# Kernel optimization log

Measured on AMD Instinct MI355X. Metric: run time of the kernel, lower is better.

## Reference

```python
import jax, jax.numpy as jnp
import numpy as np

LN_EPS = 1e-5


def setup_inputs() -> dict:
    key = jax.random.key(0)
    ks = jax.random.split(key, 8)
    dim = 256
    b, n3 = 8, 6144  # seq dim holds 3 concatenated token streams of n=2048 each
    s = 0.02
    return {
        "x": jax.random.normal(ks[0], (b, n3, dim), jnp.float32),
        "ln_g": jnp.ones((dim,), jnp.float32),
        "ln_b": jnp.zeros((dim,), jnp.float32),
        "Wq": jax.random.normal(ks[1], (dim, dim), jnp.float32) * s,
        "bq": jax.random.normal(ks[2], (dim,), jnp.float32) * s,
        "Wk": jax.random.normal(ks[3], (dim, dim), jnp.float32) * s,
        "bk": jax.random.normal(ks[4], (dim,), jnp.float32) * s,
        "Wv": jax.random.normal(ks[5], (dim, dim), jnp.float32) * s,
        "bv": jax.random.normal(ks[6], (dim,), jnp.float32) * s,
        "Wo": jax.random.normal(ks[7], (dim, dim), jnp.float32) * s,
        "bo": jnp.zeros((dim,), jnp.float32),
        "heads": 8,
    }


def reference(x, ln_g, ln_b, Wq, bq, Wk, bk, Wv, bv, Wo, bo, heads):
    dim = x.shape[-1]
    scale = dim ** (-0.5)  # NOTE: full dim, as in the original module
    d = dim // heads

    def cross_attn(xcat):
        # LayerNorm over last dim (applied to concatenated [2b, n, dim])
        mu = jnp.mean(xcat, axis=-1, keepdims=True)
        var = jnp.mean(jnp.square(xcat - mu), axis=-1, keepdims=True)
        xn = (xcat - mu) * jax.lax.rsqrt(var + LN_EPS) * ln_g + ln_b
        x1, x2 = jnp.split(xn, 2, axis=0)  # queries from stream 1, kv from stream 2
        q = x1 @ Wq.T + bq
        k = x2 @ Wk.T + bk
        v = x2 @ Wv.T + bv
        b_, n_ = q.shape[0], q.shape[1]
        q = q.reshape(b_, n_, heads, d).transpose(0, 2, 1, 3)  # b h n d
        k = k.reshape(b_, n_, heads, d).transpose(0, 2, 1, 3)
        v = v.reshape(b_, n_, heads, d).transpose(0, 2, 1, 3)
        dots = jnp.einsum('bhid,bhjd->bhij', q, k) * scale
        attn = jax.nn.softmax(dots, axis=-1)
        out = jnp.einsum('bhij,bhjd->bhid', attn, v)
        out = out.transpose(0, 2, 1, 3).reshape(b_, n_, dim)
        return out @ Wo.T + bo  # dropout is identity in eval

    x_origin, x_emap, x_lbp = jnp.split(x, 3, axis=1)
    out_oe = cross_attn(jnp.concatenate((x_origin, x_emap), axis=0))
    out_ol = cross_attn(jnp.concatenate((x_origin, x_lbp), axis=0))
    return out_oe + out_ol
```

## Files before the change

### kernel.cpp

```cpp
#include <hip/hip_runtime.h>
#include <hip/hip_bf16.h>
#include <math.h>

#define LN_EPS 1e-5f
#define QSCALE 0.09016844005556021f

typedef __attribute__((ext_vector_type(8))) short short8;
typedef __attribute__((ext_vector_type(4))) short short4v;
typedef __attribute__((ext_vector_type(4))) float f32x4;

__device__ inline ushort f2bf(float f) {
  __hip_bfloat16 h = __float2bfloat16(f);
  return *reinterpret_cast<ushort*>(&h);
}

__device__ inline uint pk2bf(float a, float b) {
  uint ua = __float_as_uint(a) + 0x8000u;
  uint ub = __float_as_uint(b) + 0x8000u;
  return __builtin_amdgcn_perm(ub, ua, 0x07060302u);
}


__global__ __launch_bounds__(256) void ln_wcast_kernel(
    const float* __restrict__ x, const float* __restrict__ lng,
    const float* __restrict__ lnb,
    const float* __restrict__ Wq, const float* __restrict__ Wk,
    const float* __restrict__ Wv, const float* __restrict__ Wo,
    ushort* __restrict__ xn, ushort* __restrict__ wbf) {
  if (blockIdx.x < 256) {
    int t = blockIdx.x * 256 + threadIdx.x;
    int e0 = t * 4;
    int m = e0 >> 16, off = e0 & 65535;
    const float* src = (m == 0) ? Wq : (m == 1) ? Wk : (m == 2) ? Wv : Wo;
    float4 v = *(const float4*)(src + off);
    ushort4 o;
    o.x = f2bf(v.x); o.y = f2bf(v.y); o.z = f2bf(v.z); o.w = f2bf(v.w);
    *(ushort4*)(wbf + m * 65536 + off) = o;
    return;
  }
  int w = threadIdx.x >> 6;
  int lane = threadIdx.x & 63;
  size_t token = (size_t)(blockIdx.x - 256) * 4 + w;
  float4 v = *(const float4*)(x + token * 256 + lane * 4);
  float s  = v.x + v.y + v.z + v.w;
  float s2 = v.x * v.x + v.y * v.y + v.z * v.z + v.w * v.w;
#pragma unroll
  for (int off = 32; off >= 1; off >>= 1) {
    s  += __shfl_xor(s, off, 64);
    s2 += __shfl_xor(s2, off, 64);
  }
  float mu  = s * (1.0f / 256.0f);
  float var = s2 * (1.0f / 256.0f) - mu * mu;
  float rs  = rsqrtf(var + LN_EPS);
  float4 g = *(const float4*)(lng + lane * 4);
  float4 bb = *(const float4*)(lnb + lane * 4);
  ushort4 o;
  o.x = f2bf((v.x - mu) * rs * g.x + bb.x);
  o.y = f2bf((v.y - mu) * rs * g.y + bb.y);
  o.z = f2bf((v.z - mu) * rs * g.z + bb.z);
  o.w = f2bf((v.w - mu) * rs * g.w + bb.w);
  *(ushort4*)(xn + token * 256 + lane * 4) = o;
}

__global__ __launch_bounds__(256) void proj_kernel(
    const ushort* __restrict__ xn,
    const ushort* __restrict__ wq, const ushort* __restrict__ wk,
    const ushort* __restrict__ wv,
    const float* __restrict__ bq, const float* __restrict__ bk,
    const float* __restrict__ bv,
    ushort* __restrict__ qb, ushort* __restrict__ keb, ushort* __restrict__ vTe,
    ushort* __restrict__ klb, ushort* __restrict__ vTl) {
  int z = blockIdx.z;
  int tid = threadIdx.x;
  int w = tid >> 6, lane = tid & 63;
  int n = lane & 15, quad = lane >> 4;
  int cbase = blockIdx.y * 128 + w * 32;
  int b = (blockIdx.x * 128) >> 11;
  int r0 = (blockIdx.x * 128) & 2047;

  if (z == 0) {
    const ushort* xbase = xn + ((size_t)b * 6144 + r0) * 256;
    short8 wf[2][8];
#pragma unroll
    for (int ct = 0; ct < 2; ++ct)
#pragma unroll
      for (int kc = 0; kc < 8; ++kc)
        wf[ct][kc] = *(const short8*)(wq + (size_t)(cbase + ct * 16 + n) * 256 + kc * 32 + quad * 8);
    float4 bt[2];
    bt[0] = *(const float4*)(bq + cbase + quad * 4);
    bt[1] = *(const float4*)(bq + cbase + 16 + quad * 4);

    short8 xfA[8], xfB[8];
#pragma unroll
    for (int kc = 0; kc < 8; ++kc)
      xfA[kc] = *(const short8*)(xbase + (size_t)n * 256 + kc * 32 + quad * 8);

#pragma unroll
    for (int tt = 0; tt < 8; ++tt) {
      const short8* cur = (tt & 1) ? xfB : xfA;
      short8* nxt = (tt & 1) ? xfA : xfB;
      if (tt < 7) {
#pragma unroll
        for (int kc = 0; kc < 8; ++kc)
          nxt[kc] = *(const short8*)(xbase + (size_t)((tt + 1) * 16 + n) * 256 + kc * 32 + quad * 8);
      }
      f32x4 acc[2] = {{0.f, 0.f, 0.f, 0.f}, {0.f, 0.f, 0.f, 0.f}};
#pragma unroll
      for (int ct = 0; ct < 2; ++ct)
#pragma unroll
        for (int kc = 0; kc < 8; ++kc)
          acc[ct] = __builtin_amdgcn_mfma_f32_16x16x32_bf16(wf[ct][kc], cur[kc], acc[ct], 0, 0, 0);
      int n2 = r0 + tt * 16 + n;
#pragma unroll
      for (int ct = 0; ct < 2; ++ct) {
        int c = cbase + ct * 16 + quad * 4;
        int h = c >> 5, d = c & 31;
        float* bp = (float*)&bt[ct];
        ushort4 st;
        st.x = f2bf((acc[ct][0] + bp[0]) * QSCALE);
        st.y = f2bf((acc[ct][1] + bp[1]) * QSCALE);
        st.z = f2bf((acc[ct][2] + bp[2]) * QSCALE);
        st.w = f2bf((acc[ct][3] + bp[3]) * QSCALE);
        *(ushort4*)(qb + (((size_t)(b * 8 + h) * 2048) + n2) * 32 + d) = st;
      }
    }
  } else {
    int s = z;
    ushort* kout = (z == 1) ? keb : klb;
    ushort* vout = (z == 1) ? vTe : vTl;
    const ushort* xbase = xn + ((size_t)b * 6144 + s * 2048 + r0) * 256;
    short8 wfk[2][8], wfv[2][8];
#pragma unroll
    for (int ct = 0; ct < 2; ++ct)
#pragma unroll
      for (int kc = 0; kc < 8; ++kc) {
        wfk[ct][kc] = *(const short8*)(wk + (size_t)(cbase + ct * 16 + n) * 256 + kc * 32 + quad * 8);
        wfv[ct][kc] = *(const short8*)(wv + (size_t)(cbase + ct * 16 + n) * 256 + kc * 32 + quad * 8);
      }
    float4 btk[2];
    btk[0] = *(const float4*)(bk + cbase + quad * 4);
    btk[1] = *(const float4*)(bk + cbase + 16 + quad * 4);
    float bsv[2] = {bv[cbase + n], bv[cbase + 16 + n]};

    short8 xfA[8], xfB[8];
#pragma unroll
    for (int kc = 0; kc < 8; ++kc)
      xfA[kc] = *(const short8*)(xbase + (size_t)n * 256 + kc * 32 + quad * 8);

#pragma unroll
    for (int tt = 0; tt < 8; ++tt) {
      const short8* cur = (tt & 1) ? xfB : xfA;
      short8* nxt = (tt & 1) ? xfA : xfB;
      if (tt < 7) {
#pragma unroll
        for (int kc = 0; kc < 8; ++kc)
          nxt[kc] = *(const short8*)(xbase + (size_t)((tt + 1) * 16 + n) * 256 + kc * 32 + quad * 8);
      }
      f32x4 ack[2] = {{0.f, 0.f, 0.f, 0.f}, {0.f, 0.f, 0.f, 0.f}};
      f32x4 acv[2] = {{0.f, 0.f, 0.f, 0.f}, {0.f, 0.f, 0.f, 0.f}};
#pragma unroll
      for (int ct = 0; ct < 2; ++ct)
#pragma unroll
        for (int kc = 0; kc < 8; ++kc) {
          ack[ct] = __builtin_amdgcn_mfma_f32_16x16x32_bf16(wfk[ct][kc], cur[kc], ack[ct], 0, 0, 0);
          acv[ct] = __builtin_amdgcn_mfma_f32_16x16x32_bf16(cur[kc], wfv[ct][kc], acv[ct], 0, 0, 0);
        }
      int n2 = r0 + tt * 16 + n;
#pragma unroll
      for (int ct = 0; ct < 2; ++ct) {
        int c = cbase + ct * 16 + quad * 4;
        int h = c >> 5, d = c & 31;
        float* bp = (float*)&btk[ct];
        ushort4 st;
        st.x = f2bf(ack[ct][0] + bp[0]);
        st.y = f2bf(ack[ct][1] + bp[1]);
        st.z = f2bf(ack[ct][2] + bp[2]);
        st.w = f2bf(ack[ct][3] + bp[3]);
        *(ushort4*)(kout + (((size_t)(b * 8 + h) * 2048) + n2) * 32 + d) = st;
      }
      int tq = r0 + tt * 16 + quad * 4;
      int tile = tq >> 6, within = tq & 63;
#pragma unroll
      for (int ct = 0; ct < 2; ++ct) {
        int c = cbase + ct * 16 + n;
        int h = c >> 5, d = c & 31;
        ushort4 st;
        st.x = f2bf(acv[ct][0] + bsv[ct]);
        st.y = f2bf(acv[ct][1] + bsv[ct]);
        st.z = f2bf(acv[ct][2] + bsv[ct]);
        st.w = f2bf(acv[ct][3] + bsv[ct]);
        *(ushort4*)(vout + (size_t)(b * 8 + h) * 65536 + tile * 2048 + d * 64 + within) = st;
      }
    }
  }
}

__global__ __launch_bounds__(256) void attn_kernel(
    const ushort* __restrict__ q,
    const ushort* __restrict__ ke, const ushort* __restrict__ vTe,
    const ushort* __restrict__ kl, const ushort* __restrict__ vTl,
    ushort* __restrict__ osum) {
  __shared__ __align__(16) short Vt[4][32 * 72];

  int tid = threadIdx.x;
  int w = tid >> 6, lane = tid & 63;
  int n = lane & 15, quad = lane >> 4;
  short* VtW = &Vt[w][0];

  union { uint2 u; short4v s; } one_u;
  one_u.u.x = 0x3F803F80u; one_u.u.y = 0x3F803F80u;
  const short4v vone = one_u.s;

  int L = blockIdx.y * 8 + blockIdx.x;
  int xcd = L & 7, idx = L >> 3;
  int bh = (idx & 7) * 8 + xcd;
  int q0 = (idx >> 3) * 256;
  int qbase = q0 + w * 64;

  short8 qfrag[4];
#pragma unroll
  for (int gq = 0; gq < 4; ++gq)
    qfrag[gq] = *(const short8*)(q + ((size_t)bh * 2048 + qbase + gq * 16 + n) * 32 + quad * 8);

  f32x4 out_acc[4][2];
#pragma unroll
  for (int gq = 0; gq < 4; ++gq)
#pragma unroll
    for (int dh = 0; dh < 2; ++dh) out_acc[gq][dh] = (f32x4){0.f, 0.f, 0.f, 0.f};

  int vrow = lane >> 3, vcol = (lane & 7) * 8;

  for (int s = 0; s < 2; ++s) {
    const ushort* K  = (s == 0 ? ke : kl) + (size_t)bh * 2048 * 32;
    const ushort* VT = (s == 0 ? vTe : vTl) + (size_t)bh * 32 * 2048;
    f32x4 lacc[4];
    f32x4 oacc[4][2];
#pragma unroll
    for (int gq = 0; gq < 4; ++gq) {
      lacc[gq] = (f32x4){0.f, 0.f, 0.f, 0.f};
#pragma unroll
      for (int dh = 0; dh < 2; ++dh) oacc[gq][dh] = (f32x4){0.f, 0.f, 0.f, 0.f};
    }

    short8 kfc[4], vrc[4], kfn[4], vrn[4];
#pragma unroll
    for (int t4 = 0; t4 < 4; ++t4)
      kfc[t4] = *(const short8*)(K + (size_t)(t4 * 16 + n) * 32 + quad * 8);
#pragma unroll
    for (int it = 0; it < 4; ++it)
      vrc[it] = *(const short8*)(VT + it * 512 + vrow * 64 + vcol);

    for (int jt = 0; jt < 32; ++jt) {
      if (jt < 31) {
        size_t tb = (size_t)(jt + 1) * 2048;
#pragma unroll
        for (int t4 = 0; t4 < 4; ++t4)
          kfn[t4] = *(const short8*)(K + tb + (size_t)(t4 * 16 + n) * 32 + quad * 8);
#pragma unroll
        for (int it = 0; it < 4; ++it)
          vrn[it] = *(const short8*)(VT + tb + it * 512 + vrow * 64 + vcol);
      }
#pragma unroll
      for (int it = 0; it < 4; ++it)
        *(short8*)&VtW[(it * 8 + vrow) * 72 + vcol] = vrc[it];
      short4v vbf[2][4];
#pragma unroll
      for (int dh = 0; dh < 2; ++dh)
#pragma unroll
        for (int t4 = 0; t4 < 4; ++t4)
          vbf[dh][t4] = *(const short4v*)&VtW[(dh * 16 + n) * 72 + t4 * 16 + quad * 4];

#pragma unroll
      for (int gq = 0; gq < 4; ++gq) {
        f32x4 sacc[4];
#pragma unroll
        for (int t4 = 0; t4 < 4; ++t4) {
          f32x4 z = {0.f, 0.f, 0.f, 0.f};
          sacc[t4] = __builtin_amdgcn_mfma_f32_16x16x32_bf16(kfc[t4], qfrag[gq], z, 0, 0, 0);
        }
        short4v pf[4];
#pragma unroll
        for (int t4 = 0; t4 < 4; ++t4) {
          float p0 = __builtin_amdgcn_exp2f(sacc[t4][0]);
          float p1 = __builtin_amdgcn_exp2f(sacc[t4][1]);
          float p2 = __builtin_amdgcn_exp2f(sacc[t4][2]);
          float p3 = __builtin_amdgcn_exp2f(sacc[t4][3]);
          union { uint2 u; short4v s4; } cv;
          cv.u.x = pk2bf(p0, p1);
          cv.u.y = pk2bf(p2, p3);
          pf[t4] = cv.s4;
        }
#pragma unroll
        for (int t4 = 0; t4 < 4; ++t4) {
          oacc[gq][0] = __builtin_amdgcn_mfma_f32_16x16x16bf16_1k(
              pf[t4], vbf[0][t4], oacc[gq][0], 0, 0, 0);
          oacc[gq][1] = __builtin_amdgcn_mfma_f32_16x16x16bf16_1k(
              pf[t4], vbf[1][t4], oacc[gq][1], 0, 0, 0);
          lacc[gq] = __builtin_amdgcn_mfma_f32_16x16x16bf16_1k(
              pf[t4], vone, lacc[gq], 0, 0, 0);
        }
      }
#pragma unroll
      for (int t4 = 0; t4 < 4; ++t4) { kfc[t4] = kfn[t4]; }
#pragma unroll
      for (int it = 0; it < 4; ++it) { vrc[it] = vrn[it]; }
    }
#pragma unroll
    for (int gq = 0; gq < 4; ++gq) {
      f32x4 inv;
#pragma unroll
      for (int r = 0; r < 4; ++r) inv[r] = __builtin_amdgcn_rcpf(lacc[gq][r]);
#pragma unroll
      for (int dh = 0; dh < 2; ++dh)
        out_acc[gq][dh] += oacc[gq][dh] * inv;
    }
  }

  int b = bh >> 3, h = bh & 7;
#pragma unroll
  for (int gq = 0; gq < 4; ++gq)
#pragma unroll
    for (int dh = 0; dh < 2; ++dh) {
      f32x4 v = out_acc[gq][dh];
#pragma unroll
      for (int r = 0; r < 4; ++r) {
        size_t row = (size_t)b * 2048 + qbase + gq * 16 + quad * 4 + r;
        osum[row * 256 + h * 32 + dh * 16 + n] = f2bf(v[r]);
      }
    }
}

__global__ __launch_bounds__(256) void outproj_kernel(
    const ushort* __restrict__ osum, const ushort* __restrict__ wo,
    const float* __restrict__ bo, float* __restrict__ out) {
  int tid = threadIdx.x;
  int w = tid >> 6, lane = tid & 63;
  int n = lane & 15, quad = lane >> 4;
  int cbase = blockIdx.y * 128 + w * 32;

  short8 wfrag[2][8];
#pragma unroll
  for (int ct = 0; ct < 2; ++ct)
#pragma unroll
    for (int kc = 0; kc < 8; ++kc)
      wfrag[ct][kc] = *(const short8*)(wo + (size_t)(cbase + ct * 16 + n) * 256 + kc * 32 + quad * 8);
  float4 bt[2];
  bt[0] = *(const float4*)(bo + cbase + quad * 4);
  bt[1] = *(const float4*)(bo + cbase + 16 + quad * 4);

  const ushort* abase = osum + (size_t)(blockIdx.x * 128) * 256;
  short8 xfA[8], xfB[8];
#pragma unroll
  for (int kc = 0; kc < 8; ++kc)
    xfA[kc] = *(const short8*)(abase + (size_t)n * 256 + kc * 32 + quad * 8);

#pragma unroll
  for (int tt = 0; tt < 8; ++tt) {
    const short8* cur = (tt & 1) ? xfB : xfA;
    short8* nxt = (tt & 1) ? xfA : xfB;
    if (tt < 7) {
#pragma unroll
      for (int kc = 0; kc < 8; ++kc)
        nxt[kc] = *(const short8*)(abase + (size_t)((tt + 1) * 16 + n) * 256 + kc * 32 + quad * 8);
    }
    int tok = blockIdx.x * 128 + tt * 16 + n;
    f32x4 acc[2] = {{0.f, 0.f, 0.f, 0.f}, {0.f, 0.f, 0.f, 0.f}};
#pragma unroll
    for (int ct = 0; ct < 2; ++ct)
#pragma unroll
      for (int kc = 0; kc < 8; ++kc)
        acc[ct] = __builtin_amdgcn_mfma_f32_16x16x32_bf16(wfrag[ct][kc], cur[kc], acc[ct], 0, 0, 0);
#pragma unroll
    for (int ct = 0; ct < 2; ++ct) {
      int c = cbase + ct * 16 + quad * 4;
      float* bp = (float*)&bt[ct];
      float4 st;
      st.x = acc[ct][0] + 2.0f * bp[0];
      st.y = acc[ct][1] + 2.0f * bp[1];
      st.z = acc[ct][2] + 2.0f * bp[2];
      st.w = acc[ct][3] + 2.0f * bp[3];
      *(float4*)(out + (size_t)tok * 256 + c) = st;
    }
  }
}

extern "C" void kernel_launch(void* const* d_in, const int* in_sizes, int n_in,
                              void* d_out, int out_size, void* d_ws, size_t ws_size,
                              hipStream_t stream) {
  const float* x   = (const float*)d_in[0];
  const float* lng = (const float*)d_in[1];
  const float* lnb = (const float*)d_in[2];
  const float* Wq  = (const float*)d_in[3];
  const float* bq  = (const float*)d_in[4];
  const float* Wk  = (const float*)d_in[5];
  const float* bk  = (const float*)d_in[6];
  const float* Wv  = (const float*)d_in[7];
  const float* bv  = (const float*)d_in[8];
  const float* Wo  = (const float*)d_in[9];
  const float* bo  = (const float*)d_in[10];
  float* out = (float*)d_out;

  ushort* ws = (ushort*)d_ws;
  const size_t XN  = (size_t)49152 * 256;
  const size_t QKV = (size_t)64 * 2048 * 32;
  ushort* xn   = ws;
  ushort* wbf  = xn + XN;
  ushort* qb   = wbf + 4 * 65536;
  ushort* keb  = qb  + QKV;
  ushort* vTe  = keb + QKV;
  ushort* klb  = vTe + QKV;
  ushort* vTl  = klb + QKV;
  ushort* osum = vTl + QKV;

  hipLaunchKernelGGL(ln_wcast_kernel, dim3(12544), dim3(256), 0, stream,
                     x, lng, lnb, Wq, Wk, Wv, Wo, xn, wbf);
  hipLaunchKernelGGL(proj_kernel, dim3(128, 2, 3), dim3(256), 0, stream,
                     xn, wbf, wbf + 65536, wbf + 131072, bq, bk, bv,
                     qb, keb, vTe, klb, vTl);
  hipLaunchKernelGGL(attn_kernel, dim3(8, 64), dim3(256), 0, stream,
                     qb, keb, vTe, klb, vTl, osum);
  hipLaunchKernelGGL(outproj_kernel, dim3(128, 2), dim3(256), 0, stream,
                     osum, wbf + 196608, bo, out);
}
```

Measured before the change: 286.4 us.

## Store V pre-swizzled into MFMA fragment order and halve per-block query tile

After: 290.8 us. Within noise of the previous version (+1.5%).

```diff
diff --git a/kernel.cpp b/kernel.cpp
--- a/kernel.cpp
+++ b/kernel.cpp
@@ -179,33 +179,34 @@
         *(ushort4*)(kout + (((size_t)(b * 8 + h) * 2048) + n2) * 32 + d) = st;
       }
       int tq = r0 + tt * 16 + quad * 4;
-      int tile = tq >> 6, within = tq & 63;
+      int tile = tq >> 6;
+      int t4 = (tq >> 4) & 3;
+      int qp = (tq >> 2) & 3;
 #pragma unroll
       for (int ct = 0; ct < 2; ++ct) {
         int c = cbase + ct * 16 + n;
         int h = c >> 5, d = c & 31;
+        int dh = d >> 4, np = d & 15;
         ushort4 st;
         st.x = f2bf(acv[ct][0] + bsv[ct]);
         st.y = f2bf(acv[ct][1] + bsv[ct]);
         st.z = f2bf(acv[ct][2] + bsv[ct]);
         st.w = f2bf(acv[ct][3] + bsv[ct]);
-        *(ushort4*)(vout + (size_t)(b * 8 + h) * 65536 + tile * 2048 + d * 64 + within) = st;
+        *(ushort4*)(vout + (size_t)(b * 8 + h) * 65536
+                    + (size_t)((((tile * 2 + dh) * 4 + t4) * 64 + qp * 16 + np) * 4)) = st;
       }
     }
   }
 }
 
-__global__ __launch_bounds__(256) void attn_kernel(
+__global__ __launch_bounds__(256, 3) void attn_kernel(
     const ushort* __restrict__ q,
     const ushort* __restrict__ ke, const ushort* __restrict__ vTe,
     const ushort* __restrict__ kl, const ushort* __restrict__ vTl,
     ushort* __restrict__ osum) {
-  __shared__ __align__(16) short Vt[4][32 * 72];
-
   int tid = threadIdx.x;
   int w = tid >> 6, lane = tid & 63;
   int n = lane & 15, quad = lane >> 4;
-  short* VtW = &Vt[w][0];
 
   union { uint2 u; short4v s; } one_u;
   one_u.u.x = 0x3F803F80u; one_u.u.y = 0x3F803F80u;
@@ -214,41 +215,42 @@
   int L = blockIdx.y * 8 + blockIdx.x;
   int xcd = L & 7, idx = L >> 3;
   int bh = (idx & 7) * 8 + xcd;
-  int q0 = (idx >> 3) * 256;
-  int qbase = q0 + w * 64;
-
-  short8 qfrag[4];
-#pragma unroll
-  for (int gq = 0; gq < 4; ++gq)
+  int q0 = (idx >> 3) * 128;
+  int qbase = q0 + w * 32;
+
+  short8 qfrag[2];
+#pragma unroll
+  for (int gq = 0; gq < 2; ++gq)
     qfrag[gq] = *(const short8*)(q + ((size_t)bh * 2048 + qbase + gq * 16 + n) * 32 + quad * 8);
 
-  f32x4 out_acc[4][2];
-#pragma unroll
-  for (int gq = 0; gq < 4; ++gq)
-#pragma unroll
-    for (int dh = 0; dh < 2; ++dh) out_acc[gq][dh] = (f32x4){0.f, 0.f, 0.f, 0.f};
-
-  int vrow = lane >> 3, vcol = (lane & 7) * 8;
+  f32x4 outv[2][2];
+#pragma unroll
+  for (int gq = 0; gq < 2; ++gq)
+#pragma unroll
+    for (int dh = 0; dh < 2; ++dh) outv[gq][dh] = (f32x4){0.f, 0.f, 0.f, 0.f};
 
   for (int s = 0; s < 2; ++s) {
     const ushort* K  = (s == 0 ? ke : kl) + (size_t)bh * 2048 * 32;
-    const ushort* VT = (s == 0 ? vTe : vTl) + (size_t)bh * 32 * 2048;
-    f32x4 lacc[4];
-    f32x4 oacc[4][2];
-#pragma unroll
-    for (int gq = 0; gq < 4; ++gq) {
+    const ushort* VT = (s == 0 ? vTe : vTl) + (size_t)bh * 65536;
+    f32x4 lacc[2];
+    f32x4 oacc[2][2];
+#pragma unroll
+    for (int gq = 0; gq < 2; ++gq) {
       lacc[gq] = (f32x4){0.f, 0.f, 0.f, 0.f};
 #pragma unroll
       for (int dh = 0; dh < 2; ++dh) oacc[gq][dh] = (f32x4){0.f, 0.f, 0.f, 0.f};
     }
 
-    short8 kfc[4], vrc[4], kfn[4], vrn[4];
+    short8 kfc[4], kfn[4];
+    short4v vfc[2][4], vfn[2][4];
 #pragma unroll
     for (int t4 = 0; t4 < 4; ++t4)
       kfc[t4] = *(const short8*)(K + (size_t)(t4 * 16 + n) * 32 + quad * 8);
 #pragma unroll
-    for (int it = 0; it < 4; ++it)
-      vrc[it] = *(const short8*)(VT + it * 512 + vrow * 64 + vcol);
+    for (int dh = 0; dh < 2; ++dh)
+#pragma unroll
+      for (int t4 = 0; t4 < 4; ++t4)
+        vfc[dh][t4] = *(const short4v*)(VT + (dh * 4 + t4) * 256 + lane * 4);
 
     for (int jt = 0; jt < 32; ++jt) {
       if (jt < 31) {
@@ -257,21 +259,13 @@
         for (int t4 = 0; t4 < 4; ++t4)
           kfn[t4] = *(const short8*)(K + tb + (size_t)(t4 * 16 + n) * 32 + quad * 8);
 #pragma unroll
-        for (int it = 0; it < 4; ++it)
-          vrn[it] = *(const short8*)(VT + tb + it * 512 + vrow * 64 + vcol);
-      }
-#pragma unroll
-      for (int it = 0; it < 4; ++it)
-        *(short8*)&VtW[(it * 8 + vrow) * 72 + vcol] = vrc[it];
-      short4v vbf[2][4];
-#pragma unroll
-      for (int dh = 0; dh < 2; ++dh)
-#pragma unroll
-        for (int t4 = 0; t4 < 4; ++t4)
-          vbf[dh][t4] = *(const short4v*)&VtW[(dh * 16 + n) * 72 + t4 * 16 + quad * 4];
-
-#pragma unroll
-      for (int gq = 0; gq < 4; ++gq) {
+        for (int dh = 0; dh < 2; ++dh)
+#pragma unroll
+          for (int t4 = 0; t4 < 4; ++t4)
+            vfn[dh][t4] = *(const short4v*)(VT + tb + (dh * 4 + t4) * 256 + lane * 4);
+      }
+#pragma unroll
+      for (int gq = 0; gq < 2; ++gq) {
         f32x4 sacc[4];
 #pragma unroll
         for (int t4 = 0; t4 < 4; ++t4) {
@@ -293,35 +287,37 @@
 #pragma unroll
         for (int t4 = 0; t4 < 4; ++t4) {
           oacc[gq][0] = __builtin_amdgcn_mfma_f32_16x16x16bf16_1k(
-              pf[t4], vbf[0][t4], oacc[gq][0], 0, 0, 0);
+              pf[t4], vfc[0][t4], oacc[gq][0], 0, 0, 0);
           oacc[gq][1] = __builtin_amdgcn_mfma_f32_16x16x16bf16_1k(
-              pf[t4], vbf[1][t4], oacc[gq][1], 0, 0, 0);
+              pf[t4], vfc[1][t4], oacc[gq][1], 0, 0, 0);
           lacc[gq] = __builtin_amdgcn_mfma_f32_16x16x16bf16_1k(
               pf[t4], vone, lacc[gq], 0, 0, 0);
         }
       }
 #pragma unroll
-      for (int t4 = 0; t4 < 4; ++t4) { kfc[t4] = kfn[t4]; }
-#pragma unroll
-      for (int it = 0; it < 4; ++it) { vrc[it] = vrn[it]; }
-    }
-#pragma unroll
-    for (int gq = 0; gq < 4; ++gq) {
+      for (int t4 = 0; t4 < 4; ++t4) kfc[t4] = kfn[t4];
+#pragma unroll
+      for (int dh = 0; dh < 2; ++dh)
+#pragma unroll
+        for (int t4 = 0; t4 < 4; ++t4) vfc[dh][t4] = vfn[dh][t4];
+    }
+#pragma unroll
+    for (int gq = 0; gq < 2; ++gq) {
       f32x4 inv;
 #pragma unroll
       for (int r = 0; r < 4; ++r) inv[r] = __builtin_amdgcn_rcpf(lacc[gq][r]);
 #pragma unroll
       for (int dh = 0; dh < 2; ++dh)
-        out_acc[gq][dh] += oacc[gq][dh] * inv;
+        outv[gq][dh] += oacc[gq][dh] * inv;
     }
   }
 
   int b = bh >> 3, h = bh & 7;
 #pragma unroll
-  for (int gq = 0; gq < 4; ++gq)
+  for (int gq = 0; gq < 2; ++gq)
 #pragma unroll
     for (int dh = 0; dh < 2; ++dh) {
-      f32x4 v = out_acc[gq][dh];
+      f32x4 v = outv[gq][dh];
 #pragma unroll
       for (int r = 0; r < 4; ++r) {
         size_t row = (size_t)b * 2048 + qbase + gq * 16 + quad * 4 + r;
@@ -417,7 +413,7 @@
   hipLaunchKernelGGL(proj_kernel, dim3(128, 2, 3), dim3(256), 0, stream,
                      xn, wbf, wbf + 65536, wbf + 131072, bq, bk, bv,
                      qb, keb, vTe, klb, vTl);
-  hipLaunchKernelGGL(attn_kernel, dim3(8, 64), dim3(256), 0, stream,
+  hipLaunchKernelGGL(attn_kernel, dim3(8, 128), dim3(256), 0, stream,
                      qb, keb, vTe, klb, vTl, osum);
   hipLaunchKernelGGL(outproj_kernel, dim3(128, 2), dim3(256), 0, stream,
                      osum, wbf + 196608, bo, out);
```
